# Kernel optimization log

Hardware: AMD Instinct MI355X
Metric: run time of the kernel (lower is better)

Reference implementation:

```python
import jax, jax.numpy as jnp
import numpy as np

EPS = 1e-5  # torch BatchNorm1d default eps

# BinActive: sign forward, straight-through estimator backward (grad clipped where |x|>1)
@jax.custom_vjp
def bin_active(x):
    return jnp.sign(x)

def _ba_fwd(x):
    return jnp.sign(x), x

def _ba_bwd(x, g):
    return (g * (jnp.abs(x) <= 1.0).astype(g.dtype),)

bin_active.defvjp(_ba_fwd, _ba_bwd)

# XNOR-style weight binarization: sign(W) * mean(|W|) per output column, STE backward
@jax.custom_vjp
def bin_weight(w):
    alpha = jnp.mean(jnp.abs(w), axis=0, keepdims=True)  # [1, out]
    return jnp.sign(w) * alpha

def _bw_fwd(w):
    alpha = jnp.mean(jnp.abs(w), axis=0, keepdims=True)
    return jnp.sign(w) * alpha, w

def _bw_bwd(w, g):
    return (g * (jnp.abs(w) <= 1.0).astype(g.dtype),)

bin_weight.defvjp(_bw_fwd, _bw_bwd)


def setup_inputs() -> dict:
    key = jax.random.key(0)
    ks = jax.random.split(key, 8)
    N, E, IN, H, OUT = 100000, 1600000, 256, 128, 40
    x = jax.random.normal(ks[0], (N, IN), dtype=jnp.float32)
    edge_index = jax.random.randint(ks[1], (2, E), 0, N, dtype=jnp.int64)
    W0 = jax.random.normal(ks[2], (IN, H), dtype=jnp.float32) * (2.0 / IN) ** 0.5
    b0 = jnp.zeros((H,), dtype=jnp.float32)
    W1 = jax.random.normal(ks[3], (H, H), dtype=jnp.float32) * (2.0 / H) ** 0.5
    b1 = jnp.zeros((H,), dtype=jnp.float32)
    W2 = jax.random.normal(ks[4], (H, OUT), dtype=jnp.float32) * (2.0 / H) ** 0.5
    b2 = jnp.zeros((OUT,), dtype=jnp.float32)
    return {"x": x, "edge_index": edge_index, "W0": W0, "b0": b0,
            "W1": W1, "b1": b1, "W2": W2, "b2": b2}


def reference(x, edge_index, W0, b0, W1, b1, W2, b2):
    n = x.shape[0]
    loop = jnp.arange(n, dtype=edge_index.dtype)
    src = jnp.concatenate([edge_index[0], loop])  # add self loops (GCN norm)
    dst = jnp.concatenate([edge_index[1], loop])
    deg = jax.ops.segment_sum(jnp.ones_like(src, dtype=x.dtype), dst, num_segments=n)
    dinv = jnp.where(deg > 0, deg ** -0.5, 0.0)
    norm = (dinv[src] * dinv[dst])[:, None]  # [E+N, 1]

    # BatchNorm1d(affine=False), training-mode batch statistics (biased var)
    mu = jnp.mean(x, axis=0)
    var = jnp.var(x, axis=0)
    h = (x - mu) * jax.lax.rsqrt(var + EPS)

    for W, b in ((W0, b0), (W1, b1), (W2, b2)):
        h = bin_active(h)                       # sign binarize (dropout skipped: eval)
        h = h @ bin_weight(W)                   # binary-weight linear
        h = jax.ops.segment_sum(h[src] * norm, dst, num_segments=n) + b  # D^-1/2 (A+I) D^-1/2 agg
    return jax.nn.log_softmax(h, axis=1)
```

## Files before the change

### kernel.cpp

```cpp
#include <hip/hip_runtime.h>
#include <math.h>

#define IN_DIM 256
#define HD 128
#define OUT_DIM 40
#define S2_STRIDE 64
#define NB_CS 1024
#define NXCD 8
#define NCHUNK 64
#define NRANGE 4
#define RMAXW 6400

__device__ __forceinline__ int xcc_id() {
    int x;
    asm volatile("s_getreg_b32 %0, hwreg(HW_REG_XCC_ID)" : "=s"(x));
    return x & (NXCD - 1);
}

__device__ __forceinline__ void nt_load4(const int* p, int* o) {
    o[0] = __builtin_nontemporal_load(p + 0);
    o[1] = __builtin_nontemporal_load(p + 1);
    o[2] = __builtin_nontemporal_load(p + 2);
    o[3] = __builtin_nontemporal_load(p + 3);
}

__global__ __launch_bounds__(256) void k_init(float* muacc8) {
    int i = blockIdx.x * 256 + threadIdx.x;
    if (i < NXCD * 256) muacc8[i] = 0.f;
}

__global__ __launch_bounds__(256) void k_fuse1(const float* __restrict__ x, int N,
                                               float* __restrict__ muacc8,
                                               const int* __restrict__ ei, int E,
                                               unsigned char* __restrict__ cntC,
                                               const float* __restrict__ W0,
                                               const float* __restrict__ W1,
                                               const float* __restrict__ W2,
                                               unsigned long long* W0p,
                                               unsigned long long* W1p,
                                               unsigned long long* W2p,
                                               float* aS0, float* aS1, float* aS2) {
    __shared__ __align__(16) unsigned ldsbuf[RMAXW];
    int b = blockIdx.x, tid = threadIdx.x;
    if (b < NB_CS) {
        float* lds = (float*)ldsbuf;
        size_t F4 = (size_t)N * (IN_DIM / 4);
        size_t stride = (size_t)NB_CS * 256;
        float a0 = 0.f, a1 = 0.f, a2 = 0.f, a3 = 0.f;
        const float4* x4 = (const float4*)x;
        for (size_t i = (size_t)b * 256 + tid; i < F4; i += stride) {
            float4 v = x4[i];
            a0 += v.x; a1 += v.y; a2 += v.z; a3 += v.w;
        }
        lds[tid] = 0.f;
        __syncthreads();
        int c0 = (tid * 4) & 255;
        atomicAdd(&lds[c0], a0);
        atomicAdd(&lds[c0 + 1], a1);
        atomicAdd(&lds[c0 + 2], a2);
        atomicAdd(&lds[c0 + 3], a3);
        __syncthreads();
        int xc = xcc_id();
        __hip_atomic_fetch_add(&muacc8[xc * 256 + tid], lds[tid],
                               __ATOMIC_RELAXED, __HIP_MEMORY_SCOPE_WORKGROUP);
    } else if (b < NB_CS + NCHUNK * NRANGE) {
        int bid2 = b - NB_CS;
        int c = bid2 >> 2, r = bid2 & (NRANGE - 1);
        for (int i = tid; i < RMAXW; i += 256) ldsbuf[i] = 0u;
        __syncthreads();
        int R = (N + NRANGE - 1) / NRANGE;
        int base = r * R;
        int lim = N - base; if (lim > R) lim = R; if (lim < 0) lim = 0;
        int chunk = ((E + NCHUNK - 1) / NCHUNK + 3) & ~3;
        int eBeg = c * chunk, eEnd = E < eBeg + chunk ? E : eBeg + chunk;
        const int* dptr = ei + E;
        int e = eBeg;
        if ((((unsigned)(E + eBeg)) & 3u) == 0 && eBeg < eEnd) {
            int n4 = (eEnd - eBeg) >> 2;
            for (int i = tid; i < n4; i += 256) {
                int dd[4];
                nt_load4(dptr + eBeg + 4 * i, dd);
                unsigned r0 = (unsigned)(dd[0] - base);
                unsigned r1 = (unsigned)(dd[1] - base);
                unsigned r2 = (unsigned)(dd[2] - base);
                unsigned r3 = (unsigned)(dd[3] - base);
                if (r0 < (unsigned)lim) atomicAdd(&ldsbuf[r0 >> 2], 1u << (8 * (r0 & 3)));
                if (r1 < (unsigned)lim) atomicAdd(&ldsbuf[r1 >> 2], 1u << (8 * (r1 & 3)));
                if (r2 < (unsigned)lim) atomicAdd(&ldsbuf[r2 >> 2], 1u << (8 * (r2 & 3)));
                if (r3 < (unsigned)lim) atomicAdd(&ldsbuf[r3 >> 2], 1u << (8 * (r3 & 3)));
            }
            e = eBeg + (n4 << 2);
        }
        for (e += tid; e < eEnd; e += 256) {
            unsigned rel = (unsigned)(dptr[e] - base);
            if (rel < (unsigned)lim) atomicAdd(&ldsbuf[rel >> 2], 1u << (8 * (rel & 3)));
        }
        __syncthreads();
        for (int i = tid; i < lim; i += 256) {
            unsigned cv = (ldsbuf[i >> 2] >> (8 * (i & 3))) & 0xFFu;
            cntC[(size_t)c * N + base + i] = (unsigned char)cv;
        }
    } else {
        int b2 = b - NB_CS - NCHUNK * NRANGE;
        int lane = tid & 63, w = tid >> 6;
        if (b2 < 32) {
            int j = b2 * 4 + w;
            float asum = 0.f;
            unsigned long long words[4];
            #pragma unroll
            for (int q = 0; q < 4; ++q) {
                float v = W0[(size_t)(4 * lane + q) * HD + j];
                asum += fabsf(v);
                words[q] = __ballot(v < 0.f);
            }
            #pragma unroll
            for (int off = 32; off; off >>= 1) asum += __shfl_xor(asum, off);
            if (lane == 0) {
                aS0[j] = 2.f * asum / 256.f;
                #pragma unroll
                for (int q = 0; q < 4; ++q) W0p[j * 4 + q] = words[q];
            }
        } else if (b2 < 64) {
            int j = (b2 - 32) * 4 + w;
            int fl = lane & 15, kk = lane >> 4;
            float asum = 0.f;
            unsigned long long words[2];
            #pragma unroll
            for (int q = 0; q < 2; ++q) {
                float v = W1[(size_t)(fl * 8 + 4 * q + kk) * HD + j];
                asum += fabsf(v);
                words[q] = __ballot(v < 0.f);
            }
            #pragma unroll
            for (int off = 32; off; off >>= 1) asum += __shfl_xor(asum, off);
            if (lane == 0) {
                aS1[j] = 2.f * asum / 128.f;
                W1p[j * 2 + 0] = words[0];
                W1p[j * 2 + 1] = words[1];
            }
        } else {
            int j = (b2 - 64) * 4 + w;
            int fl = lane & 15, kk = lane >> 4;
            if (j < OUT_DIM) {
                float asum = 0.f;
                unsigned long long words[2];
                #pragma unroll
                for (int q = 0; q < 2; ++q) {
                    float v = W2[(size_t)(fl * 8 + 4 * q + kk) * OUT_DIM + j];
                    asum += fabsf(v);
                    words[q] = __ballot(v < 0.f);
                }
                #pragma unroll
                for (int off = 32; off; off >>= 1) asum += __shfl_xor(asum, off);
                if (lane == 0) {
                    aS2[j] = 2.f * asum / 128.f;
                    W2p[j * 2 + 0] = words[0];
                    W2p[j * 2 + 1] = words[1];
                }
            }
        }
    }
}

__global__ __launch_bounds__(256) void k_bp(unsigned char* __restrict__ cntC, int N,
                                            int* bp, float* __restrict__ dinv,
                                            int* __restrict__ cnt) {
    __shared__ int sm[256];
    int i = blockIdx.x * 256 + threadIdx.x;
    int c = 0;
    if (i < N) {
        int run = 0;
        #pragma unroll
        for (int h = 0; h < NCHUNK; ++h) {
            unsigned bc = cntC[(size_t)h * N + i];
            cntC[(size_t)h * N + i] = (unsigned char)run;
            run += (int)bc;
        }
        c = run;
        cnt[i] = run;
        dinv[i] = (float)(1.0 / sqrt((double)(run + 1)));
    }
    sm[threadIdx.x] = c;
    __syncthreads();
    for (int off = 128; off; off >>= 1) {
        if (threadIdx.x < off) sm[threadIdx.x] += sm[threadIdx.x + off];
        __syncthreads();
    }
    if (threadIdx.x == 0) bp[blockIdx.x] = sm[0];
}

__global__ __launch_bounds__(512) void k_scanbp(const int* __restrict__ bp, int NB, int* bps,
                                                const float* __restrict__ muacc8,
                                                float* __restrict__ mu) {
    __shared__ int sm[512];
    int t = threadIdx.x;
    if (t < 256) {
        float s = 0.f;
        #pragma unroll
        for (int xc = 0; xc < NXCD; ++xc) s += muacc8[xc * 256 + t];
        mu[t] = s;
    }
    int v = (t < NB) ? bp[t] : 0;
    sm[t] = v;
    __syncthreads();
    for (int off = 1; off < 512; off <<= 1) {
        int add = (t >= off) ? sm[t - off] : 0;
        __syncthreads();
        sm[t] += add;
        __syncthreads();
    }
    if (t < NB) bps[t] = sm[t] - v;
}

__global__ __launch_bounds__(256) void k_rowptr(const int* __restrict__ cnt,
                                                const int* __restrict__ bps, int N, int E,
                                                int* row_ptr) {
    __shared__ int wsum[4];
    int t = threadIdx.x, lane = t & 63, w = t >> 6;
    int i = blockIdx.x * 256 + t;
    int c = (i < N) ? cnt[i] : 0;
    int v = c;
    #pragma unroll
    for (int off = 1; off < 64; off <<= 1) {
        int n = __shfl_up(v, off);
        if (lane >= off) v += n;
    }
    if (lane == 63) wsum[w] = v;
    __syncthreads();
    int wo = 0;
    for (int k = 0; k < w; ++k) wo += wsum[k];
    int excl = bps[blockIdx.x] + wo + v - c;
    if (i < N) row_ptr[i] = excl;
    if (blockIdx.x == 0 && t == 0) row_ptr[N] = E;
}

__global__ __launch_bounds__(256) void k_fuse2(const int* __restrict__ ei, int E,
                                               const int* __restrict__ rowp,
                                               const unsigned char* __restrict__ xoffC,
                                               int* __restrict__ cs4,
                                               const float* __restrict__ x,
                                               const float* __restrict__ muacc, float inv_n,
                                               const unsigned long long* __restrict__ W0p,
                                               unsigned char* __restrict__ S0, int N) {
    __shared__ __align__(16) unsigned sh32[RMAXW];
    int b = blockIdx.x, tid = threadIdx.x;
    if (b < NCHUNK * NRANGE) {
        int c = b >> 2, r = b & (NRANGE - 1);
        for (int i = tid; i < RMAXW; i += 256) sh32[i] = 0u;
        __syncthreads();
        int R = (N + NRANGE - 1) / NRANGE;
        int base = r * R;
        int lim = N - base; if (lim > R) lim = R; if (lim < 0) lim = 0;
        int chunk = ((E + NCHUNK - 1) / NCHUNK + 3) & ~3;
        int eBeg = c * chunk, eEnd = E < eBeg + chunk ? E : eBeg + chunk;
        int e = eBeg;
        if (((unsigned)eBeg & 3u) == 0 && (((unsigned)(E + eBeg)) & 3u) == 0 && eBeg < eEnd) {
            int n4 = (eEnd - eBeg) >> 2;
            for (int i = tid; i < n4; i += 256) {
                int ss[4], dd[4];
                nt_load4(ei + eBeg + 4 * i, ss);
                nt_load4(ei + E + eBeg + 4 * i, dd);
                #pragma unroll
                for (int k = 0; k < 4; ++k) {
                    unsigned rel = (unsigned)(dd[k] - base);
                    if (rel < (unsigned)lim) {
                        unsigned old = atomicAdd(&sh32[rel >> 2], 1u << (8 * (rel & 3)));
                        int lr = (int)((old >> (8 * (rel & 3))) & 0xFFu);
                        int pos = rowp[dd[k]] +
                                  (int)xoffC[(size_t)c * N + dd[k]] + lr;
                        cs4[pos] = ss[k];
                    }
                }
            }
            e = eBeg + (n4 << 2);
        }
        for (e += tid; e < eEnd; e += 256) {
            int d = ei[E + e];
            unsigned rel = (unsigned)(d - base);
            if (rel < (unsigned)lim) {
                unsigned old = atomicAdd(&sh32[rel >> 2], 1u << (8 * (rel & 3)));
                int lr = (int)((old >> (8 * (rel & 3))) & 0xFFu);
                int pos = rowp[d] + (int)xoffC[(size_t)c * N + d] + lr;
                cs4[pos] = ei[e];
            }
        }
    } else {
        unsigned long long* w0s = (unsigned long long*)sh32;
        {
            int i = tid;
            w0s[9 * (i >> 3) + (i & 7)] = W0p[i];
            i = tid + 256;
            w0s[9 * (i >> 3) + (i & 7)] = W0p[i];
        }
        __syncthreads();
        int lane = tid & 63;
        int row = (b - NCHUNK * NRANGE) * 4 + (tid >> 6);
        if (row >= N) return;
        float4 xv = ((const float4*)(x + (size_t)row * IN_DIM))[lane];
        float4 ms = ((const float4*)muacc)[lane];
        unsigned long long xw[4];
        xw[0] = __ballot(xv.x < ms.x * inv_n);
        xw[1] = __ballot(xv.y < ms.y * inv_n);
        xw[2] = __ballot(xv.z < ms.z * inv_n);
        xw[3] = __ballot(xv.w < ms.w * inv_n);
        unsigned int pack = 0;
        #pragma unroll
        for (int t2 = 0; t2 < 2; ++t2) {
            const unsigned long long* wc = &w0s[9 * lane + 4 * t2];
            int dd = __popcll(xw[0] ^ wc[0]) + __popcll(xw[1] ^ wc[1]) +
                     __popcll(xw[2] ^ wc[2]) + __popcll(xw[3] ^ wc[3]);
            int S = IN_DIM - 2 * dd;
            int s8 = S >> 1;
            if (s8 > 127) s8 = 127;
            pack |= ((unsigned int)(s8 + 128) & 0xffu) << (8 * t2);
        }
        *(unsigned short*)(S0 + (size_t)row * HD + 2 * lane) = (unsigned short)pack;
    }
}

__device__ __forceinline__ void acc4s(float n, unsigned v, float* a) {
    a[0] = fmaf(n, (float)(v & 0xffu) - 128.f, a[0]);
    a[1] = fmaf(n, (float)((v >> 8) & 0xffu) - 128.f, a[1]);
    a[2] = fmaf(n, (float)((v >> 16) & 0xffu) - 128.f, a[2]);
    a[3] = fmaf(n, (float)(v >> 24) - 128.f, a[3]);
}

template <int OUTC>
__global__ __launch_bounds__(256) void k_agg_mm(const unsigned char* __restrict__ Sin,
                                                const int* __restrict__ row_ptr,
                                                const int* __restrict__ cs4,
                                                const float* __restrict__ dinv,
                                                const float* __restrict__ alphaS,
                                                const float* __restrict__ bias,
                                                const unsigned long long* __restrict__ Wnp,
                                                unsigned char* __restrict__ Sout, int N) {
    __shared__ unsigned long long wsm[OUTC * 2 + OUTC / 4 + 8];
    int tid = threadIdx.x;
    for (int i = tid; i < OUTC * 2; i += 256) wsm[9 * (i >> 3) + (i & 7)] = Wnp[i];
    __syncthreads();
    int lane = tid & 63;
    int d = blockIdx.x * 4 + (tid >> 6);
    if (d >= N) return;
    int sub = lane >> 4;
    int fl  = lane & 15;
    float dv = dinv[d];
    float acc[8];
    #pragma unroll
    for (int k = 0; k < 8; ++k) acc[k] = 0.f;
    if (sub == 0) {
        float nrm = dv * dv;
        unsigned long long rr = *(const unsigned long long*)(Sin + (size_t)d * HD + fl * 8);
        acc4s(nrm, (unsigned)rr, acc);
        acc4s(nrm, (unsigned)(rr >> 32), acc + 4);
    }
    int e0 = row_ptr[d], e1 = row_ptr[d + 1];
    int e = e0 + sub;
    for (; e + 12 < e1; e += 16) {
        int s0_ = cs4[e], s1_ = cs4[e + 4], s2_ = cs4[e + 8], s3_ = cs4[e + 12];
        float n0 = dinv[s0_] * dv, n1 = dinv[s1_] * dv;
        float n2 = dinv[s2_] * dv, n3 = dinv[s3_] * dv;
        unsigned long long r0 = *(const unsigned long long*)(Sin + (size_t)s0_ * HD + fl * 8);
        unsigned long long r1 = *(const unsigned long long*)(Sin + (size_t)s1_ * HD + fl * 8);
        unsigned long long r2 = *(const unsigned long long*)(Sin + (size_t)s2_ * HD + fl * 8);
        unsigned long long r3 = *(const unsigned long long*)(Sin + (size_t)s3_ * HD + fl * 8);
        acc4s(n0, (unsigned)r0, acc); acc4s(n0, (unsigned)(r0 >> 32), acc + 4);
        acc4s(n1, (unsigned)r1, acc); acc4s(n1, (unsigned)(r1 >> 32), acc + 4);
        acc4s(n2, (unsigned)r2, acc); acc4s(n2, (unsigned)(r2 >> 32), acc + 4);
        acc4s(n3, (unsigned)r3, acc); acc4s(n3, (unsigned)(r3 >> 32), acc + 4);
    }
    for (; e + 4 < e1; e += 8) {
        int sa = cs4[e], sb = cs4[e + 4];
        float na = dinv[sa] * dv, nb = dinv[sb] * dv;
        unsigned long long ra = *(const unsigned long long*)(Sin + (size_t)sa * HD + fl * 8);
        unsigned long long rb = *(const unsigned long long*)(Sin + (size_t)sb * HD + fl * 8);
        acc4s(na, (unsigned)ra, acc); acc4s(na, (unsigned)(ra >> 32), acc + 4);
        acc4s(nb, (unsigned)rb, acc); acc4s(nb, (unsigned)(rb >> 32), acc + 4);
    }
    if (e < e1) {
        int s = cs4[e];
        float nrm = dinv[s] * dv;
        unsigned long long rr = *(const unsigned long long*)(Sin + (size_t)s * HD + fl * 8);
        acc4s(nrm, (unsigned)rr, acc);
        acc4s(nrm, (unsigned)(rr >> 32), acc + 4);
    }
    #pragma unroll
    for (int k = 0; k < 8; ++k) {
        acc[k] += __shfl_xor(acc[k], 16);
        acc[k] += __shfl_xor(acc[k], 32);
    }
    unsigned int m8 = 0;
    #pragma unroll
    for (int k = 0; k < 8; ++k) {
        int f = fl * 8 + k;
        float v = alphaS[f] * acc[k] + bias[f];
        if (v < 0.f) m8 |= (1u << k);
    }
    unsigned long long x0 = 0, x1 = 0;
    #pragma unroll
    for (int k = 0; k < 4; ++k) {
        unsigned long long bk = __ballot((m8 >> k) & 1u);
        x0 |= (bk & 0xffffULL) << (16 * k);
    }
    #pragma unroll
    for (int k = 4; k < 8; ++k) {
        unsigned long long bk = __ballot((m8 >> k) & 1u);
        x1 |= (bk & 0xffffULL) << (16 * (k - 4));
    }
    if (OUTC == 128) {
        unsigned int pack = 0;
        #pragma unroll
        for (int t2 = 0; t2 < 2; ++t2) {
            int j = 2 * lane + t2;
            int i0 = j * 2;
            const unsigned long long* wc = &wsm[9 * (i0 >> 3) + (i0 & 7)];
            int dd = __popcll(x0 ^ wc[0]) + __popcll(x1 ^ wc[1]);
            int S = HD - 2 * dd;
            pack |= ((unsigned int)((S >> 1) + 128) & 0xffu) << (8 * t2);
        }
        *(unsigned short*)(Sout + (size_t)d * HD + 2 * lane) = (unsigned short)pack;
    } else {
        int p8 = 128;
        if (lane < OUTC) {
            int i0 = lane * 2;
            const unsigned long long* wc = &wsm[9 * (i0 >> 3) + (i0 & 7)];
            int dd = __popcll(x0 ^ wc[0]) + __popcll(x1 ^ wc[1]);
            p8 = ((HD - 2 * dd) >> 1) + 128;
        }
        Sout[(size_t)d * S2_STRIDE + lane] = (unsigned char)p8;
    }
}

__global__ __launch_bounds__(256) void k_agg_out(const unsigned char* __restrict__ S2,
                                                 const int* __restrict__ row_ptr,
                                                 const int* __restrict__ cs4,
                                                 const float* __restrict__ dinv,
                                                 const float* __restrict__ alphaS2,
                                                 const float* __restrict__ b2,
                                                 float* __restrict__ out, int N) {
    int tid = threadIdx.x, lane = tid & 63;
    int d = blockIdx.x * 4 + (tid >> 6);
    if (d >= N) return;
    int sub = lane >> 4;
    int fl  = lane & 15;
    float dv = dinv[d];
    float acc[4] = {0.f, 0.f, 0.f, 0.f};
    if (sub == 0) {
        float nrm = dv * dv;
        unsigned int r4 = *(const unsigned int*)(S2 + (size_t)d * S2_STRIDE + fl * 4);
        acc4s(nrm, r4, acc);
    }
    int e0 = row_ptr[d], e1 = row_ptr[d + 1];
    int e = e0 + sub;
    for (; e + 12 < e1; e += 16) {
        int s0_ = cs4[e], s1_ = cs4[e + 4], s2_ = cs4[e + 8], s3_ = cs4[e + 12];
        float n0 = dinv[s0_] * dv, n1 = dinv[s1_] * dv;
        float n2 = dinv[s2_] * dv, n3 = dinv[s3_] * dv;
        unsigned int r0 = *(const unsigned int*)(S2 + (size_t)s0_ * S2_STRIDE + fl * 4);
        unsigned int r1 = *(const unsigned int*)(S2 + (size_t)s1_ * S2_STRIDE + fl * 4);
        unsigned int r2 = *(const unsigned int*)(S2 + (size_t)s2_ * S2_STRIDE + fl * 4);
        unsigned int r3 = *(const unsigned int*)(S2 + (size_t)s3_ * S2_STRIDE + fl * 4);
        acc4s(n0, r0, acc);
        acc4s(n1, r1, acc);
        acc4s(n2, r2, acc);
        acc4s(n3, r3, acc);
    }
    for (; e + 4 < e1; e += 8) {
        int sa = cs4[e], sb = cs4[e + 4];
        float na = dinv[sa] * dv, nb = dinv[sb] * dv;
        unsigned int ra = *(const unsigned int*)(S2 + (size_t)sa * S2_STRIDE + fl * 4);
        unsigned int rb = *(const unsigned int*)(S2 + (size_t)sb * S2_STRIDE + fl * 4);
        acc4s(na, ra, acc);
        acc4s(nb, rb, acc);
    }
    if (e < e1) {
        int s = cs4[e];
        float nrm = dinv[s] * dv;
        unsigned int r4 = *(const unsigned int*)(S2 + (size_t)s * S2_STRIDE + fl * 4);
        acc4s(nrm, r4, acc);
    }
    #pragma unroll
    for (int k = 0; k < 4; ++k) {
        acc[k] += __shfl_xor(acc[k], 16);
        acc[k] += __shfl_xor(acc[k], 32);
    }
    float h[4];
    float mymax = -INFINITY;
    #pragma unroll
    for (int k = 0; k < 4; ++k) {
        int f = fl * 4 + k;
        h[k] = (f < OUT_DIM) ? (alphaS2[f] * acc[k] + b2[f]) : -INFINITY;
        mymax = fmaxf(mymax, h[k]);
    }
    #pragma unroll
    for (int off = 1; off < 16; off <<= 1) mymax = fmaxf(mymax, __shfl_xor(mymax, off));
    float s4 = 0.f;
    #pragma unroll
    for (int k = 0; k < 4; ++k) {
        if (fl * 4 + k < OUT_DIM) s4 += expf(h[k] - mymax);
    }
    #pragma unroll
    for (int off = 1; off < 16; off <<= 1) s4 += __shfl_xor(s4, off);
    float lse = mymax + logf(s4);
    if (sub == 0 && fl < OUT_DIM / 4) {
        float4 o;
        o.x = h[0] - lse; o.y = h[1] - lse; o.z = h[2] - lse; o.w = h[3] - lse;
        *(float4*)(out + (size_t)d * OUT_DIM + fl * 4) = o;
    }
}

extern "C" void kernel_launch(void* const* d_in, const int* in_sizes, int n_in,
                              void* d_out, int out_size, void* d_ws, size_t ws_size,
                              hipStream_t stream) {
    const float* x  = (const float*)d_in[0];
    const int*   ei = (const int*)d_in[1];
    const float* W0 = (const float*)d_in[2];
    const float* b0 = (const float*)d_in[3];
    const float* W1 = (const float*)d_in[4];
    const float* b1 = (const float*)d_in[5];
    const float* W2 = (const float*)d_in[6];
    const float* b2 = (const float*)d_in[7];
    float* out = (float*)d_out;

    int N = in_sizes[0] / IN_DIM;
    int E = in_sizes[1] / 2;

    char* ws = (char*)d_ws;
    size_t off = 0;
    auto alloc = [&](size_t bytes) -> void* {
        off = (off + 255) & ~(size_t)255;
        void* p = (void*)(ws + off);
        off += bytes;
        return p;
    };
    float* mu     = (float*)alloc(256 * 4);
    float* muacc8 = (float*)alloc(NXCD * 256 * 4);
    unsigned char* cntC = (unsigned char*)alloc((size_t)NCHUNK * N);
    int*   cnt    = (int*)alloc((size_t)N * 4);
    float* dinv   = (float*)alloc((size_t)N * 4);
    int*   rowp   = (int*)alloc(((size_t)N + 1) * 4);
    int*   bp     = (int*)alloc(512 * 4);
    int*   bps    = (int*)alloc(512 * 4);
    int*   cs4    = (int*)alloc((size_t)E * 4);
    unsigned char* S0 = (unsigned char*)alloc((size_t)N * HD);
    unsigned char* S1 = (unsigned char*)alloc((size_t)N * HD);
    unsigned char* S2 = (unsigned char*)alloc((size_t)N * S2_STRIDE);
    unsigned long long* W0p = (unsigned long long*)alloc(128 * 4 * 8);
    unsigned long long* W1p = (unsigned long long*)alloc(128 * 2 * 8);
    unsigned long long* W2p = (unsigned long long*)alloc(40 * 2 * 8);
    float* aS0 = (float*)alloc(128 * 4);
    float* aS1 = (float*)alloc(128 * 4);
    float* aS2 = (float*)alloc(40 * 4);

    int nb256 = (N + 255) / 256;
    float inv_n = 1.0f / (float)N;

    k_init<<<dim3(8), dim3(256), 0, stream>>>(muacc8);
    k_fuse1<<<dim3(NB_CS + NCHUNK * NRANGE + 74), dim3(256), 0, stream>>>(
        x, N, muacc8, ei, E, cntC, W0, W1, W2, W0p, W1p, W2p, aS0, aS1, aS2);
    k_bp<<<dim3(nb256), dim3(256), 0, stream>>>(cntC, N, bp, dinv, cnt);
    k_scanbp<<<dim3(1), dim3(512), 0, stream>>>(bp, nb256, bps, muacc8, mu);
    k_rowptr<<<dim3(nb256), dim3(256), 0, stream>>>(cnt, bps, N, E, rowp);

    int nb4 = (N + 3) / 4;
    k_fuse2<<<dim3(NCHUNK * NRANGE + nb4), dim3(256), 0, stream>>>(
        ei, E, rowp, cntC, cs4, x, mu, inv_n, W0p, S0, N);
    k_agg_mm<128><<<dim3(nb4), dim3(256), 0, stream>>>(S0, rowp, cs4, dinv, aS0, b0, W1p, S1, N);
    k_agg_mm<40><<<dim3(nb4), dim3(256), 0, stream>>>(S1, rowp, cs4, dinv, aS1, b1, W2p, S2, N);
    k_agg_out<<<dim3(nb4), dim3(256), 0, stream>>>(S2, rowp, cs4, dinv, aS2, b2, out, N);
    (void)out_size; (void)ws_size; (void)n_in;
}
```

Measured before the change: 479.0 us.

## Use 16 node ranges with 16-bit LDS counters and 32-bit gather addressing

The edge-count and CSR-scatter phases now split nodes into 16 ranges instead of 4 and keep 16-bit packed counters in a smaller LDS buffer. This cuts LDS per block and adds more blocks, but each block still reads its whole edge chunk, so edge traffic rises fourfold. Separately, the aggregation kernels compute gather addresses with 32-bit shifts instead of 64-bit multiplies to save address arithmetic. The per-chunk count is still stored as a byte, so the wider counter adds no range.

```diff
diff --git a/kernel.cpp b/kernel.cpp
--- a/kernel.cpp
+++ b/kernel.cpp
@@ -8,8 +8,8 @@
 #define NB_CS 1024
 #define NXCD 8
 #define NCHUNK 64
-#define NRANGE 4
-#define RMAXW 6400
+#define NRANGE 16
+#define RMAXW 3200
 
 __device__ __forceinline__ int xcc_id() {
     int x;
@@ -65,7 +65,7 @@
                                __ATOMIC_RELAXED, __HIP_MEMORY_SCOPE_WORKGROUP);
     } else if (b < NB_CS + NCHUNK * NRANGE) {
         int bid2 = b - NB_CS;
-        int c = bid2 >> 2, r = bid2 & (NRANGE - 1);
+        int c = bid2 >> 4, r = bid2 & (NRANGE - 1);
         for (int i = tid; i < RMAXW; i += 256) ldsbuf[i] = 0u;
         __syncthreads();
         int R = (N + NRANGE - 1) / NRANGE;
@@ -84,20 +84,20 @@
                 unsigned r1 = (unsigned)(dd[1] - base);
                 unsigned r2 = (unsigned)(dd[2] - base);
                 unsigned r3 = (unsigned)(dd[3] - base);
-                if (r0 < (unsigned)lim) atomicAdd(&ldsbuf[r0 >> 2], 1u << (8 * (r0 & 3)));
-                if (r1 < (unsigned)lim) atomicAdd(&ldsbuf[r1 >> 2], 1u << (8 * (r1 & 3)));
-                if (r2 < (unsigned)lim) atomicAdd(&ldsbuf[r2 >> 2], 1u << (8 * (r2 & 3)));
-                if (r3 < (unsigned)lim) atomicAdd(&ldsbuf[r3 >> 2], 1u << (8 * (r3 & 3)));
+                if (r0 < (unsigned)lim) atomicAdd(&ldsbuf[r0 >> 1], 1u << (16 * (r0 & 1)));
+                if (r1 < (unsigned)lim) atomicAdd(&ldsbuf[r1 >> 1], 1u << (16 * (r1 & 1)));
+                if (r2 < (unsigned)lim) atomicAdd(&ldsbuf[r2 >> 1], 1u << (16 * (r2 & 1)));
+                if (r3 < (unsigned)lim) atomicAdd(&ldsbuf[r3 >> 1], 1u << (16 * (r3 & 1)));
             }
             e = eBeg + (n4 << 2);
         }
         for (e += tid; e < eEnd; e += 256) {
             unsigned rel = (unsigned)(dptr[e] - base);
-            if (rel < (unsigned)lim) atomicAdd(&ldsbuf[rel >> 2], 1u << (8 * (rel & 3)));
+            if (rel < (unsigned)lim) atomicAdd(&ldsbuf[rel >> 1], 1u << (16 * (rel & 1)));
         }
         __syncthreads();
         for (int i = tid; i < lim; i += 256) {
-            unsigned cv = (ldsbuf[i >> 2] >> (8 * (i & 3))) & 0xFFu;
+            unsigned cv = (ldsbuf[i >> 1] >> (16 * (i & 1))) & 0xFFFFu;
             cntC[(size_t)c * N + base + i] = (unsigned char)cv;
         }
     } else {
@@ -245,7 +245,7 @@
     __shared__ __align__(16) unsigned sh32[RMAXW];
     int b = blockIdx.x, tid = threadIdx.x;
     if (b < NCHUNK * NRANGE) {
-        int c = b >> 2, r = b & (NRANGE - 1);
+        int c = b >> 4, r = b & (NRANGE - 1);
         for (int i = tid; i < RMAXW; i += 256) sh32[i] = 0u;
         __syncthreads();
         int R = (N + NRANGE - 1) / NRANGE;
@@ -264,8 +264,8 @@
                 for (int k = 0; k < 4; ++k) {
                     unsigned rel = (unsigned)(dd[k] - base);
                     if (rel < (unsigned)lim) {
-                        unsigned old = atomicAdd(&sh32[rel >> 2], 1u << (8 * (rel & 3)));
-                        int lr = (int)((old >> (8 * (rel & 3))) & 0xFFu);
+                        unsigned old = atomicAdd(&sh32[rel >> 1], 1u << (16 * (rel & 1)));
+                        int lr = (int)((old >> (16 * (rel & 1))) & 0xFFFFu);
                         int pos = rowp[dd[k]] +
                                   (int)xoffC[(size_t)c * N + dd[k]] + lr;
                         cs4[pos] = ss[k];
@@ -278,8 +278,8 @@
             int d = ei[E + e];
             unsigned rel = (unsigned)(d - base);
             if (rel < (unsigned)lim) {
-                unsigned old = atomicAdd(&sh32[rel >> 2], 1u << (8 * (rel & 3)));
-                int lr = (int)((old >> (8 * (rel & 3))) & 0xFFu);
+                unsigned old = atomicAdd(&sh32[rel >> 1], 1u << (16 * (rel & 1)));
+                int lr = (int)((old >> (16 * (rel & 1))) & 0xFFFFu);
                 int pos = rowp[d] + (int)xoffC[(size_t)c * N + d] + lr;
                 cs4[pos] = ei[e];
             }
@@ -342,14 +342,14 @@
     int d = blockIdx.x * 4 + (tid >> 6);
     if (d >= N) return;
     int sub = lane >> 4;
-    int fl  = lane & 15;
+    unsigned fl8 = ((unsigned)lane & 15) * 8;
     float dv = dinv[d];
     float acc[8];
     #pragma unroll
     for (int k = 0; k < 8; ++k) acc[k] = 0.f;
     if (sub == 0) {
         float nrm = dv * dv;
-        unsigned long long rr = *(const unsigned long long*)(Sin + (size_t)d * HD + fl * 8);
+        unsigned long long rr = *(const unsigned long long*)(Sin + (((unsigned)d << 7) + fl8));
         acc4s(nrm, (unsigned)rr, acc);
         acc4s(nrm, (unsigned)(rr >> 32), acc + 4);
     }
@@ -359,10 +359,10 @@
         int s0_ = cs4[e], s1_ = cs4[e + 4], s2_ = cs4[e + 8], s3_ = cs4[e + 12];
         float n0 = dinv[s0_] * dv, n1 = dinv[s1_] * dv;
         float n2 = dinv[s2_] * dv, n3 = dinv[s3_] * dv;
-        unsigned long long r0 = *(const unsigned long long*)(Sin + (size_t)s0_ * HD + fl * 8);
-        unsigned long long r1 = *(const unsigned long long*)(Sin + (size_t)s1_ * HD + fl * 8);
-        unsigned long long r2 = *(const unsigned long long*)(Sin + (size_t)s2_ * HD + fl * 8);
-        unsigned long long r3 = *(const unsigned long long*)(Sin + (size_t)s3_ * HD + fl * 8);
+        unsigned long long r0 = *(const unsigned long long*)(Sin + (((unsigned)s0_ << 7) + fl8));
+        unsigned long long r1 = *(const unsigned long long*)(Sin + (((unsigned)s1_ << 7) + fl8));
+        unsigned long long r2 = *(const unsigned long long*)(Sin + (((unsigned)s2_ << 7) + fl8));
+        unsigned long long r3 = *(const unsigned long long*)(Sin + (((unsigned)s3_ << 7) + fl8));
         acc4s(n0, (unsigned)r0, acc); acc4s(n0, (unsigned)(r0 >> 32), acc + 4);
         acc4s(n1, (unsigned)r1, acc); acc4s(n1, (unsigned)(r1 >> 32), acc + 4);
         acc4s(n2, (unsigned)r2, acc); acc4s(n2, (unsigned)(r2 >> 32), acc + 4);
@@ -371,15 +371,15 @@
     for (; e + 4 < e1; e += 8) {
         int sa = cs4[e], sb = cs4[e + 4];
         float na = dinv[sa] * dv, nb = dinv[sb] * dv;
-        unsigned long long ra = *(const unsigned long long*)(Sin + (size_t)sa * HD + fl * 8);
-        unsigned long long rb = *(const unsigned long long*)(Sin + (size_t)sb * HD + fl * 8);
+        unsigned long long ra = *(const unsigned long long*)(Sin + (((unsigned)sa << 7) + fl8));
+        unsigned long long rb = *(const unsigned long long*)(Sin + (((unsigned)sb << 7) + fl8));
         acc4s(na, (unsigned)ra, acc); acc4s(na, (unsigned)(ra >> 32), acc + 4);
         acc4s(nb, (unsigned)rb, acc); acc4s(nb, (unsigned)(rb >> 32), acc + 4);
     }
     if (e < e1) {
         int s = cs4[e];
         float nrm = dinv[s] * dv;
-        unsigned long long rr = *(const unsigned long long*)(Sin + (size_t)s * HD + fl * 8);
+        unsigned long long rr = *(const unsigned long long*)(Sin + (((unsigned)s << 7) + fl8));
         acc4s(nrm, (unsigned)rr, acc);
         acc4s(nrm, (unsigned)(rr >> 32), acc + 4);
     }
@@ -391,7 +391,7 @@
     unsigned int m8 = 0;
     #pragma unroll
     for (int k = 0; k < 8; ++k) {
-        int f = fl * 8 + k;
+        unsigned f = fl8 + k;
         float v = alphaS[f] * acc[k] + bias[f];
         if (v < 0.f) m8 |= (1u << k);
     }
@@ -417,7 +417,7 @@
             int S = HD - 2 * dd;
             pack |= ((unsigned int)((S >> 1) + 128) & 0xffu) << (8 * t2);
         }
-        *(unsigned short*)(Sout + (size_t)d * HD + 2 * lane) = (unsigned short)pack;
+        *(unsigned short*)(Sout + (((unsigned)d << 7) + 2 * (unsigned)lane)) = (unsigned short)pack;
     } else {
         int p8 = 128;
         if (lane < OUTC) {
@@ -426,7 +426,7 @@
             int dd = __popcll(x0 ^ wc[0]) + __popcll(x1 ^ wc[1]);
             p8 = ((HD - 2 * dd) >> 1) + 128;
         }
-        Sout[(size_t)d * S2_STRIDE + lane] = (unsigned char)p8;
+        Sout[((unsigned)d << 6) + (unsigned)lane] = (unsigned char)p8;
     }
 }
 
@@ -441,12 +441,12 @@
     int d = blockIdx.x * 4 + (tid >> 6);
     if (d >= N) return;
     int sub = lane >> 4;
-    int fl  = lane & 15;
+    unsigned fl4 = ((unsigned)lane & 15) * 4;
     float dv = dinv[d];
     float acc[4] = {0.f, 0.f, 0.f, 0.f};
     if (sub == 0) {
         float nrm = dv * dv;
-        unsigned int r4 = *(const unsigned int*)(S2 + (size_t)d * S2_STRIDE + fl * 4);
+        unsigned int r4 = *(const unsigned int*)(S2 + (((unsigned)d << 6) + fl4));
         acc4s(nrm, r4, acc);
     }
     int e0 = row_ptr[d], e1 = row_ptr[d + 1];
@@ -455,10 +455,10 @@
         int s0_ = cs4[e], s1_ = cs4[e + 4], s2_ = cs4[e + 8], s3_ = cs4[e + 12];
         float n0 = dinv[s0_] * dv, n1 = dinv[s1_] * dv;
         float n2 = dinv[s2_] * dv, n3 = dinv[s3_] * dv;
-        unsigned int r0 = *(const unsigned int*)(S2 + (size_t)s0_ * S2_STRIDE + fl * 4);
-        unsigned int r1 = *(const unsigned int*)(S2 + (size_t)s1_ * S2_STRIDE + fl * 4);
-        unsigned int r2 = *(const unsigned int*)(S2 + (size_t)s2_ * S2_STRIDE + fl * 4);
-        unsigned int r3 = *(const unsigned int*)(S2 + (size_t)s3_ * S2_STRIDE + fl * 4);
+        unsigned int r0 = *(const unsigned int*)(S2 + (((unsigned)s0_ << 6) + fl4));
+        unsigned int r1 = *(const unsigned int*)(S2 + (((unsigned)s1_ << 6) + fl4));
+        unsigned int r2 = *(const unsigned int*)(S2 + (((unsigned)s2_ << 6) + fl4));
+        unsigned int r3 = *(const unsigned int*)(S2 + (((unsigned)s3_ << 6) + fl4));
         acc4s(n0, r0, acc);
         acc4s(n1, r1, acc);
         acc4s(n2, r2, acc);
@@ -467,15 +467,15 @@
     for (; e + 4 < e1; e += 8) {
         int sa = cs4[e], sb = cs4[e + 4];
         float na = dinv[sa] * dv, nb = dinv[sb] * dv;
-        unsigned int ra = *(const unsigned int*)(S2 + (size_t)sa * S2_STRIDE + fl * 4);
-        unsigned int rb = *(const unsigned int*)(S2 + (size_t)sb * S2_STRIDE + fl * 4);
+        unsigned int ra = *(const unsigned int*)(S2 + (((unsigned)sa << 6) + fl4));
+        unsigned int rb = *(const unsigned int*)(S2 + (((unsigned)sb << 6) + fl4));
         acc4s(na, ra, acc);
         acc4s(nb, rb, acc);
     }
     if (e < e1) {
         int s = cs4[e];
         float nrm = dinv[s] * dv;
-        unsigned int r4 = *(const unsigned int*)(S2 + (size_t)s * S2_STRIDE + fl * 4);
+        unsigned int r4 = *(const unsigned int*)(S2 + (((unsigned)s << 6) + fl4));
         acc4s(nrm, r4, acc);
     }
     #pragma unroll
@@ -487,7 +487,7 @@
     float mymax = -INFINITY;
     #pragma unroll
     for (int k = 0; k < 4; ++k) {
-        int f = fl * 4 + k;
+        int f = (int)fl4 + k;
         h[k] = (f < OUT_DIM) ? (alphaS2[f] * acc[k] + b2[f]) : -INFINITY;
         mymax = fmaxf(mymax, h[k]);
     }
@@ -496,15 +496,15 @@
     float s4 = 0.f;
     #pragma unroll
     for (int k = 0; k < 4; ++k) {
-        if (fl * 4 + k < OUT_DIM) s4 += expf(h[k] - mymax);
+        if ((int)fl4 + k < OUT_DIM) s4 += expf(h[k] - mymax);
     }
     #pragma unroll
     for (int off = 1; off < 16; off <<= 1) s4 += __shfl_xor(s4, off);
     float lse = mymax + logf(s4);
-    if (sub == 0 && fl < OUT_DIM / 4) {
+    if (sub == 0 && (int)fl4 < OUT_DIM) {
         float4 o;
         o.x = h[0] - lse; o.y = h[1] - lse; o.z = h[2] - lse; o.w = h[3] - lse;
-        *(float4*)(out + (size_t)d * OUT_DIM + fl * 4) = o;
+        *(float4*)(out + (size_t)d * OUT_DIM + fl4) = o;
     }
 }
 
```

Result: slower. 501.7 us (+4.7%).
